# Kernel tuning notes

Hardware: AMD Instinct MI355X
Metric: run time of the kernel (lower is better)

## Reference

```python
import jax, jax.numpy as jnp
import numpy as np

LN_EPS = 1e-5


def _ssm_scan(x_ssm, A, Bm, C, reverse):
    # x_ssm: [B, L, d_inner]; A, Bm, C: [d_inner, d_state]
    Bb, L, di = x_ssm.shape
    ds = Bm.shape[1]

    def step(h, x_t):
        # h: [B, d_inner, d_state], x_t: [B, d_inner]
        h = jnp.clip(h * A[None] + x_t[:, :, None] * Bm[None], -10.0, 10.0)
        y = jnp.einsum('bid,id->bi', h, C)
        return h, y

    h0 = jnp.zeros((Bb, di, ds), x_ssm.dtype)
    _, ys = jax.lax.scan(step, h0, jnp.swapaxes(x_ssm, 0, 1), reverse=reverse)
    return jnp.swapaxes(ys, 0, 1)  # [B, L, d_inner], time-ordered


def setup_inputs() -> dict:
    key = jax.random.key(0)
    ks = jax.random.split(key, 6)
    B, L, D = 4, 2048, 1024
    d_state, expand = 16, 2
    d_inner = D * expand
    x = jax.random.normal(ks[0], (B, L, D), jnp.float32)
    # xavier-ish scaled params
    in_proj_w = jax.random.normal(ks[1], (d_inner * 2, D), jnp.float32) * np.float32(1.0 / np.sqrt(D))
    A_log = jax.random.normal(ks[2], (d_inner, d_state), jnp.float32)
    B_mat = jax.random.normal(ks[3], (d_inner, d_state), jnp.float32) * np.float32(1.0 / np.sqrt(d_state))
    C_mat = jnp.full((d_inner, d_state), 0.01, jnp.float32)
    out_proj_w = jax.random.normal(ks[4], (D, d_inner), jnp.float32) * np.float32(1.0 / np.sqrt(d_inner))
    ln_w = jnp.ones((D,), jnp.float32)
    ln_b = jnp.zeros((D,), jnp.float32)
    return {"x": x, "in_proj_w": in_proj_w, "A_log": A_log, "B_mat": B_mat,
            "C_mat": C_mat, "out_proj_w": out_proj_w, "ln_w": ln_w, "ln_b": ln_b}


def reference(x, in_proj_w, A_log, B_mat, C_mat, out_proj_w, ln_w, ln_b):
    # LayerNorm
    mu = jnp.mean(x, axis=-1, keepdims=True)
    var = jnp.mean((x - mu) ** 2, axis=-1, keepdims=True)
    xn = (x - mu) * jax.lax.rsqrt(var + LN_EPS) * ln_w + ln_b
    # in_proj (no bias), split into ssm stream and gate
    x_proj = jnp.einsum('bld,ed->ble', xn, in_proj_w)  # [B, L, 2*d_inner]
    x_ssm, gate = jnp.split(x_proj, 2, axis=-1)
    # A = -clamp(exp(A_log), -10, -0.01)  (saturates to 0.01, kept faithfully)
    A = -jnp.clip(jnp.exp(A_log), -10.0, -0.01)
    out_f = _ssm_scan(x_ssm, A, B_mat, C_mat, reverse=False)
    out_b = _ssm_scan(x_ssm, A, B_mat, C_mat, reverse=True)
    out = (out_f + out_b) * 0.5 * jax.nn.silu(gate)
    return jnp.einsum('bli,di->bld', out, out_proj_w)
```

## Files before the change

### kernel.cpp

```cpp
#include <hip/hip_runtime.h>

typedef __attribute__((ext_vector_type(8))) _Float16 f16x8;
typedef __attribute__((ext_vector_type(4))) float f32x4;

#define GLOBAL_AS __attribute__((address_space(1)))
#define LDS_AS __attribute__((address_space(3)))

static constexpr int Bb = 4, LL = 2048, DD = 1024, DI = 2048, DS = 16;
static constexpr int MROWS = Bb * LL;
static constexpr int N1 = 2 * DI;
static constexpr int K1 = DD;
static constexpr int N2 = DD;
static constexpr int K2 = DI;

__device__ __forceinline__ unsigned short f2h(float f) {
  _Float16 h = (_Float16)f;
  union { _Float16 h; unsigned short u; } c; c.h = h;
  return c.u;
}
__device__ __forceinline__ float h2f(unsigned short u) {
  union { unsigned short u; _Float16 h; } c; c.u = u;
  return (float)c.h;
}

__global__ __launch_bounds__(256) void ln_half_kernel(
    const float* __restrict__ x, const float* __restrict__ lnw,
    const float* __restrict__ lnb, unsigned short* __restrict__ A1) {
  const int r = blockIdx.x;
  const int tid = threadIdx.x;
  const float4 v = reinterpret_cast<const float4*>(x + (size_t)r * DD)[tid];
  float s = v.x + v.y + v.z + v.w;
#pragma unroll
  for (int off = 32; off >= 1; off >>= 1) s += __shfl_xor(s, off, 64);
  __shared__ float red[8];
  const int wid = tid >> 6;
  if ((tid & 63) == 0) red[wid] = s;
  __syncthreads();
  const float mu = (red[0] + red[1] + red[2] + red[3]) * (1.0f / DD);
  const float dx = v.x - mu, dy = v.y - mu, dz = v.z - mu, dw = v.w - mu;
  float ss = dx * dx + dy * dy + dz * dz + dw * dw;
#pragma unroll
  for (int off = 32; off >= 1; off >>= 1) ss += __shfl_xor(ss, off, 64);
  if ((tid & 63) == 0) red[4 + wid] = ss;
  __syncthreads();
  const float var = (red[4] + red[5] + red[6] + red[7]) * (1.0f / DD);
  const float rs = rsqrtf(var + 1e-5f);
  const float4 w4 = reinterpret_cast<const float4*>(lnw)[tid];
  const float4 b4 = reinterpret_cast<const float4*>(lnb)[tid];
  ushort4 h4;
  h4.x = f2h(dx * rs * w4.x + b4.x);
  h4.y = f2h(dy * rs * w4.y + b4.y);
  h4.z = f2h(dz * rs * w4.z + b4.z);
  h4.w = f2h(dw * rs * w4.w + b4.w);
  *reinterpret_cast<ushort4*>(&A1[(size_t)r * DD + tid * 4]) = h4;
}

__global__ __launch_bounds__(256) void f32_to_f16_kernel(
    const float* __restrict__ W, unsigned short* __restrict__ O) {
  const int gid = blockIdx.x * 256 + threadIdx.x;
  const float4 w = reinterpret_cast<const float4*>(W)[gid];
  ushort4 h4;
  h4.x = f2h(w.x); h4.y = f2h(w.y); h4.z = f2h(w.z); h4.w = f2h(w.w);
  reinterpret_cast<ushort4*>(O)[gid] = h4;
}

__global__ __launch_bounds__(512, 2) void gemm_bt_256(
    const unsigned short* __restrict__ A, const unsigned short* __restrict__ B,
    unsigned short* __restrict__ C, int M, int N, int K) {
  __shared__ unsigned short sm[2][2][256 * 64];
  const int tid = threadIdx.x;
  const int wid = tid >> 6;
  const int lane = tid & 63;
  const int wm = wid >> 2;
  const int wn = wid & 3;
  const int mt = M >> 8;
  const int cpx = gridDim.x >> 3;
  const int bid = blockIdx.x;
  const int sw = (bid & 7) * cpx + (bid >> 3);
  const int bm = sw % mt;
  const int bn = sw / mt;
  const size_t arow0 = (size_t)bm * 256;
  const size_t brow0 = (size_t)bn * 256;

  const unsigned short* gA[4];
  const unsigned short* gB[4];
#pragma unroll
  for (int j = 0; j < 4; ++j) {
    const int idx = j * 512 + tid;
    const int prow = idx >> 3;
    const int scol = ((idx & 7) ^ (prow & 7)) << 3;
    gA[j] = A + (arow0 + prow) * (size_t)K + scol;
    gB[j] = B + (brow0 + prow) * (size_t)K + scol;
  }
  auto stageA = [&](int buf) {
#pragma unroll
    for (int j = 0; j < 4; ++j) {
      __builtin_amdgcn_global_load_lds((const GLOBAL_AS void*)gA[j],
          (LDS_AS void*)&sm[buf][0][(j * 512 + (wid << 6)) * 8], 16, 0, 0);
      gA[j] += 64;
    }
  };
  auto stageB = [&](int buf) {
#pragma unroll
    for (int j = 0; j < 4; ++j) {
      __builtin_amdgcn_global_load_lds((const GLOBAL_AS void*)gB[j],
          (LDS_AS void*)&sm[buf][1][(j * 512 + (wid << 6)) * 8], 16, 0, 0);
      gB[j] += 64;
    }
  };

  const int q = lane >> 4;
  const int l7 = lane & 7;
  const int fr = lane & 15;
  int swz[2];
  swz[0] = (q << 3) ^ (l7 << 3);
  swz[1] = (32 + (q << 3)) ^ (l7 << 3);

  int arows[8], brows[4];
#pragma unroll
  for (int mf = 0; mf < 8; ++mf) arows[mf] = ((wm << 7) + mf * 16 + fr) * 64;
#pragma unroll
  for (int nf = 0; nf < 4; ++nf) brows[nf] = ((wn << 6) + nf * 16 + fr) * 64;

  f32x4 acc[8][4] = {};

  const int NTK = K >> 6;
  stageA(0);
  stageB(0);
  asm volatile("s_waitcnt vmcnt(0)" ::: "memory");
  __builtin_amdgcn_s_barrier();

  for (int t = 0; t < NTK; ++t) {
    const int cur = t & 1, nxt = cur ^ 1;
    const bool more = (t + 1 < NTK);
    f16x8 aF[4][2], bL[2][2], bH[2][2];
#pragma unroll
    for (int mf = 0; mf < 4; ++mf)
#pragma unroll
      for (int ks = 0; ks < 2; ++ks)
        aF[mf][ks] = *reinterpret_cast<const f16x8*>(&sm[cur][0][arows[mf] + swz[ks]]);
#pragma unroll
    for (int nf = 0; nf < 2; ++nf)
#pragma unroll
      for (int ks = 0; ks < 2; ++ks)
        bL[nf][ks] = *reinterpret_cast<const f16x8*>(&sm[cur][1][brows[nf] + swz[ks]]);
    if (more) stageA(nxt);
    __builtin_amdgcn_s_barrier();
    asm volatile("s_waitcnt lgkmcnt(0)" ::: "memory");
    __builtin_amdgcn_sched_barrier(0);
    __builtin_amdgcn_s_setprio(1);
#pragma unroll
    for (int mf = 0; mf < 4; ++mf)
#pragma unroll
      for (int nf = 0; nf < 2; ++nf)
#pragma unroll
        for (int ks = 0; ks < 2; ++ks)
          acc[mf][nf] = __builtin_amdgcn_mfma_f32_16x16x32_f16(
              aF[mf][ks], bL[nf][ks], acc[mf][nf], 0, 0, 0);
    __builtin_amdgcn_s_setprio(0);
    __builtin_amdgcn_s_barrier();
#pragma unroll
    for (int nf = 0; nf < 2; ++nf)
#pragma unroll
      for (int ks = 0; ks < 2; ++ks)
        bH[nf][ks] = *reinterpret_cast<const f16x8*>(&sm[cur][1][brows[2 + nf] + swz[ks]]);
    if (more) stageB(nxt);
    __builtin_amdgcn_s_barrier();
    asm volatile("s_waitcnt lgkmcnt(0)" ::: "memory");
    __builtin_amdgcn_sched_barrier(0);
    __builtin_amdgcn_s_setprio(1);
#pragma unroll
    for (int mf = 0; mf < 4; ++mf)
#pragma unroll
      for (int nf = 0; nf < 2; ++nf)
#pragma unroll
        for (int ks = 0; ks < 2; ++ks)
          acc[mf][2 + nf] = __builtin_amdgcn_mfma_f32_16x16x32_f16(
              aF[mf][ks], bH[nf][ks], acc[mf][2 + nf], 0, 0, 0);
    __builtin_amdgcn_s_setprio(0);
    __builtin_amdgcn_s_barrier();
#pragma unroll
    for (int mf = 0; mf < 4; ++mf)
#pragma unroll
      for (int ks = 0; ks < 2; ++ks)
        aF[mf][ks] = *reinterpret_cast<const f16x8*>(&sm[cur][0][arows[4 + mf] + swz[ks]]);
    __builtin_amdgcn_s_barrier();
    asm volatile("s_waitcnt lgkmcnt(0)" ::: "memory");
    __builtin_amdgcn_sched_barrier(0);
    __builtin_amdgcn_s_setprio(1);
#pragma unroll
    for (int mf = 0; mf < 4; ++mf)
#pragma unroll
      for (int nf = 0; nf < 2; ++nf)
#pragma unroll
        for (int ks = 0; ks < 2; ++ks)
          acc[4 + mf][2 + nf] = __builtin_amdgcn_mfma_f32_16x16x32_f16(
              aF[mf][ks], bH[nf][ks], acc[4 + mf][2 + nf], 0, 0, 0);
    __builtin_amdgcn_s_setprio(0);
    __builtin_amdgcn_s_barrier();
    __builtin_amdgcn_s_setprio(1);
#pragma unroll
    for (int mf = 0; mf < 4; ++mf)
#pragma unroll
      for (int nf = 0; nf < 2; ++nf)
#pragma unroll
        for (int ks = 0; ks < 2; ++ks)
          acc[4 + mf][nf] = __builtin_amdgcn_mfma_f32_16x16x32_f16(
              aF[mf][ks], bL[nf][ks], acc[4 + mf][nf], 0, 0, 0);
    __builtin_amdgcn_s_setprio(0);
    if (more) asm volatile("s_waitcnt vmcnt(0)" ::: "memory");
    __builtin_amdgcn_s_barrier();
  }

  const int fcol = lane & 15;
  const int frow4 = (lane >> 4) << 2;
#pragma unroll
  for (int mf = 0; mf < 8; ++mf)
#pragma unroll
    for (int nf = 0; nf < 4; ++nf) {
      const size_t row0 = arow0 + (wm << 7) + mf * 16 + frow4;
      const size_t col = brow0 + (wn << 6) + nf * 16 + fcol;
#pragma unroll
      for (int j = 0; j < 4; ++j)
        C[(row0 + j) * (size_t)N + col] = f2h(acc[mf][nf][j]);
    }
}

__global__ __launch_bounds__(256) void gemm_bt(
    const unsigned short* __restrict__ A, const unsigned short* __restrict__ B,
    float* __restrict__ C, int M, int N, int K) {
  __shared__ unsigned short lA[128 * 32];
  __shared__ unsigned short lB[128 * 32];
  const int tid = threadIdx.x;
  const int wid = tid >> 6;
  const int lane = tid & 63;
  const size_t arow0 = (size_t)blockIdx.x * 128;
  const size_t brow0 = (size_t)blockIdx.y * 128;
  const int wr = wid >> 1, wc = wid & 1;
  f32x4 acc[4][4] = {};

  const int idx0 = tid, idx1 = 256 + tid;
  const unsigned short* ga0 = A + (arow0 + (idx0 >> 2)) * K + (idx0 & 3) * 8;
  const unsigned short* ga1 = A + (arow0 + (idx1 >> 2)) * K + (idx1 & 3) * 8;
  const unsigned short* gb0 = B + (brow0 + (idx0 >> 2)) * K + (idx0 & 3) * 8;
  const unsigned short* gb1 = B + (brow0 + (idx1 >> 2)) * K + (idx1 & 3) * 8;
  const int lb0 = (wid * 64) * 8;
  const int lb1 = (256 + wid * 64) * 8;

  for (int k0 = 0; k0 < K; k0 += 32) {
    __builtin_amdgcn_global_load_lds((const GLOBAL_AS void*)(ga0 + k0),
                                     (LDS_AS void*)(&lA[lb0]), 16, 0, 0);
    __builtin_amdgcn_global_load_lds((const GLOBAL_AS void*)(ga1 + k0),
                                     (LDS_AS void*)(&lA[lb1]), 16, 0, 0);
    __builtin_amdgcn_global_load_lds((const GLOBAL_AS void*)(gb0 + k0),
                                     (LDS_AS void*)(&lB[lb0]), 16, 0, 0);
    __builtin_amdgcn_global_load_lds((const GLOBAL_AS void*)(gb1 + k0),
                                     (LDS_AS void*)(&lB[lb1]), 16, 0, 0);
    __syncthreads();
    const int fr = lane & 15;
    const int fo = (lane >> 4) * 8;
    f16x8 af[4], bfr[4];
#pragma unroll
    for (int m = 0; m < 4; ++m)
      af[m] = *reinterpret_cast<const f16x8*>(&lA[(wr * 64 + m * 16 + fr) * 32 + fo]);
#pragma unroll
    for (int n = 0; n < 4; ++n)
      bfr[n] = *reinterpret_cast<const f16x8*>(&lB[(wc * 64 + n * 16 + fr) * 32 + fo]);
#pragma unroll
    for (int m = 0; m < 4; ++m)
#pragma unroll
      for (int n = 0; n < 4; ++n)
        acc[m][n] = __builtin_amdgcn_mfma_f32_16x16x32_f16(af[m], bfr[n], acc[m][n], 0, 0, 0);
    __syncthreads();
  }
  const int fcol = lane & 15;
  const int frow = (lane >> 4) * 4;
#pragma unroll
  for (int m = 0; m < 4; ++m)
#pragma unroll
    for (int n = 0; n < 4; ++n)
#pragma unroll
      for (int j = 0; j < 4; ++j) {
        const size_t row = arow0 + wr * 64 + m * 16 + frow + j;
        const size_t col = brow0 + wc * 64 + n * 16 + fcol;
        C[row * (size_t)N + col] = acc[m][n][j];
      }
}

__global__ __launch_bounds__(256) void scan_kernel(
    const unsigned short* __restrict__ xp, const float* __restrict__ Bm,
    const float* __restrict__ Cm, unsigned short* __restrict__ oss) {
  constexpr int T = 32, KH = 8;
  const int blk = blockIdx.x;
  const int igrp = blk & 7;
  const int c = (blk >> 3) & 63;
  const int b = blk >> 9;
  const int tid = threadIdx.x;
  const int i = igrp * 256 + tid;
  float d = 0.f;
  {
    const float4* bp = reinterpret_cast<const float4*>(Bm + (size_t)i * DS);
    const float4* cp = reinterpret_cast<const float4*>(Cm + (size_t)i * DS);
#pragma unroll
    for (int qv = 0; qv < 4; ++qv) {
      const float4 bv = bp[qv], cv = cp[qv];
      d += bv.x * cv.x + bv.y * cv.y + bv.z * cv.z + bv.w * cv.w;
    }
  }
  const float dh = 0.5f * d;
  const int t0 = c * T;
  const size_t rowbase = (size_t)b * LL;
  float yf[T];
  float g = 0.f;
  {
    const int hstart = (t0 >= KH) ? t0 - KH : 0;
    for (int t = hstart; t < t0; ++t)
      g = fmaf(0.01f, g, h2f(xp[(rowbase + t) * (size_t)N1 + i]));
#pragma unroll
    for (int j = 0; j < T; ++j) {
      g = fmaf(0.01f, g, h2f(xp[(rowbase + t0 + j) * (size_t)N1 + i]));
      yf[j] = g;
    }
  }
  g = 0.f;
  {
    const int tend = (t0 + T - 1 + KH <= LL - 1) ? (t0 + T - 1 + KH) : (LL - 1);
    for (int t = tend; t >= t0 + T; --t)
      g = fmaf(0.01f, g, h2f(xp[(rowbase + t) * (size_t)N1 + i]));
#pragma unroll
    for (int j = T - 1; j >= 0; --j) {
      const size_t row = rowbase + t0 + j;
      g = fmaf(0.01f, g, h2f(xp[row * (size_t)N1 + i]));
      const float gt = h2f(xp[row * (size_t)N1 + DI + i]);
      const float sg = gt / (1.f + expf(-gt));
      const float o = (yf[j] + g) * dh * sg;
      oss[row * (size_t)DI + i] = f2h(o);
    }
  }
}

extern "C" void kernel_launch(void* const* d_in, const int* in_sizes, int n_in,
                              void* d_out, int out_size, void* d_ws, size_t ws_size,
                              hipStream_t stream) {
  (void)in_sizes; (void)n_in; (void)out_size; (void)ws_size;
  const float* x          = (const float*)d_in[0];
  const float* in_proj_w  = (const float*)d_in[1];
  const float* B_mat      = (const float*)d_in[3];
  const float* C_mat      = (const float*)d_in[4];
  const float* out_proj_w = (const float*)d_in[5];
  const float* ln_w       = (const float*)d_in[6];
  const float* ln_b       = (const float*)d_in[7];
  float* out = (float*)d_out;

  char* ws = (char*)d_ws;
  unsigned short* A1  = (unsigned short*)ws; ws += (size_t)MROWS * K1 * 2;
  unsigned short* B1  = (unsigned short*)ws; ws += (size_t)N1 * K1 * 2;
  unsigned short* B2  = (unsigned short*)ws; ws += (size_t)N2 * K2 * 2;
  unsigned short* OSS = (unsigned short*)ws; ws += (size_t)MROWS * DI * 2;
  unsigned short* XP  = (unsigned short*)ws; ws += (size_t)MROWS * N1 * 2;

  f32_to_f16_kernel<<<dim3((N1 * K1 / 4) / 256), dim3(256), 0, stream>>>(in_proj_w, B1);
  f32_to_f16_kernel<<<dim3((N2 * K2 / 4) / 256), dim3(256), 0, stream>>>(out_proj_w, B2);
  ln_half_kernel<<<dim3(MROWS), dim3(256), 0, stream>>>(x, ln_w, ln_b, A1);
  gemm_bt_256<<<dim3((MROWS / 256) * (N1 / 256)), dim3(512), 0, stream>>>(A1, B1, XP, MROWS, N1, K1);
  scan_kernel<<<dim3(2048), dim3(256), 0, stream>>>(XP, B_mat, C_mat, OSS);
  gemm_bt<<<dim3(MROWS / 128, N2 / 128), dim3(256), 0, stream>>>(OSS, B2, out, MROWS, N2, K2);
}
```

Baseline: 194.4 us.

## Replace out_proj GEMM with double-buffered 256x128 tile kernel with swizzled LDS

The output-projection GEMM moves from a simple 128x128 single-buffer kernel to a 512-thread 256x128 tile kernel. It double-buffers LDS, prefetching the next K=64 slice while MFMAs run on the current one. It also uses an XOR-swizzled LDS layout to avoid bank conflicts, staged barriers with setprio, and a swizzled block order for L2 locality. The aim is to hide global-load latency and raise MFMA utilisation, at the cost of more LDS per block and fewer blocks in flight.

Result: no change. 191.0 us (-1.7%).

```diff
diff --git a/kernel.cpp b/kernel.cpp
--- a/kernel.cpp
+++ b/kernel.cpp
@@ -226,65 +226,160 @@
     }
 }
 
-__global__ __launch_bounds__(256) void gemm_bt(
+__global__ __launch_bounds__(512, 2) void gemm_bt_256n128(
     const unsigned short* __restrict__ A, const unsigned short* __restrict__ B,
     float* __restrict__ C, int M, int N, int K) {
-  __shared__ unsigned short lA[128 * 32];
-  __shared__ unsigned short lB[128 * 32];
+  __shared__ unsigned short sm[2][24576];
   const int tid = threadIdx.x;
   const int wid = tid >> 6;
   const int lane = tid & 63;
-  const size_t arow0 = (size_t)blockIdx.x * 128;
-  const size_t brow0 = (size_t)blockIdx.y * 128;
-  const int wr = wid >> 1, wc = wid & 1;
-  f32x4 acc[4][4] = {};
-
-  const int idx0 = tid, idx1 = 256 + tid;
-  const unsigned short* ga0 = A + (arow0 + (idx0 >> 2)) * K + (idx0 & 3) * 8;
-  const unsigned short* ga1 = A + (arow0 + (idx1 >> 2)) * K + (idx1 & 3) * 8;
-  const unsigned short* gb0 = B + (brow0 + (idx0 >> 2)) * K + (idx0 & 3) * 8;
-  const unsigned short* gb1 = B + (brow0 + (idx1 >> 2)) * K + (idx1 & 3) * 8;
-  const int lb0 = (wid * 64) * 8;
-  const int lb1 = (256 + wid * 64) * 8;
-
-  for (int k0 = 0; k0 < K; k0 += 32) {
-    __builtin_amdgcn_global_load_lds((const GLOBAL_AS void*)(ga0 + k0),
-                                     (LDS_AS void*)(&lA[lb0]), 16, 0, 0);
-    __builtin_amdgcn_global_load_lds((const GLOBAL_AS void*)(ga1 + k0),
-                                     (LDS_AS void*)(&lA[lb1]), 16, 0, 0);
-    __builtin_amdgcn_global_load_lds((const GLOBAL_AS void*)(gb0 + k0),
-                                     (LDS_AS void*)(&lB[lb0]), 16, 0, 0);
-    __builtin_amdgcn_global_load_lds((const GLOBAL_AS void*)(gb1 + k0),
-                                     (LDS_AS void*)(&lB[lb1]), 16, 0, 0);
-    __syncthreads();
-    const int fr = lane & 15;
-    const int fo = (lane >> 4) * 8;
-    f16x8 af[4], bfr[4];
-#pragma unroll
-    for (int m = 0; m < 4; ++m)
-      af[m] = *reinterpret_cast<const f16x8*>(&lA[(wr * 64 + m * 16 + fr) * 32 + fo]);
-#pragma unroll
-    for (int n = 0; n < 4; ++n)
-      bfr[n] = *reinterpret_cast<const f16x8*>(&lB[(wc * 64 + n * 16 + fr) * 32 + fo]);
-#pragma unroll
-    for (int m = 0; m < 4; ++m)
-#pragma unroll
-      for (int n = 0; n < 4; ++n)
-        acc[m][n] = __builtin_amdgcn_mfma_f32_16x16x32_f16(af[m], bfr[n], acc[m][n], 0, 0, 0);
-    __syncthreads();
-  }
+  const int wm = wid >> 2;
+  const int wn = wid & 3;
+  const int mt = M >> 8;
+  const int cpx = gridDim.x >> 3;
+  const int bid = blockIdx.x;
+  const int sw = (bid & 7) * cpx + (bid >> 3);
+  const int bm = sw % mt;
+  const int bn = sw / mt;
+  const size_t arow0 = (size_t)bm * 256;
+  const size_t brow0 = (size_t)bn * 128;
+
+  const unsigned short* gA[4];
+  const unsigned short* gB[2];
+#pragma unroll
+  for (int j = 0; j < 4; ++j) {
+    const int idx = j * 512 + tid;
+    const int prow = idx >> 3;
+    const int scol = ((idx & 7) ^ (prow & 7)) << 3;
+    gA[j] = A + (arow0 + prow) * (size_t)K + scol;
+  }
+#pragma unroll
+  for (int j = 0; j < 2; ++j) {
+    const int idx = j * 512 + tid;
+    const int prow = idx >> 3;
+    const int scol = ((idx & 7) ^ (prow & 7)) << 3;
+    gB[j] = B + (brow0 + prow) * (size_t)K + scol;
+  }
+  auto stageA = [&](int buf) {
+#pragma unroll
+    for (int j = 0; j < 4; ++j) {
+      __builtin_amdgcn_global_load_lds((const GLOBAL_AS void*)gA[j],
+          (LDS_AS void*)&sm[buf][(j * 512 + (wid << 6)) * 8], 16, 0, 0);
+      gA[j] += 64;
+    }
+  };
+  auto stageB = [&](int buf) {
+#pragma unroll
+    for (int j = 0; j < 2; ++j) {
+      __builtin_amdgcn_global_load_lds((const GLOBAL_AS void*)gB[j],
+          (LDS_AS void*)&sm[buf][16384 + (j * 512 + (wid << 6)) * 8], 16, 0, 0);
+      gB[j] += 64;
+    }
+  };
+
+  const int q = lane >> 4;
+  const int l7 = lane & 7;
+  const int fr = lane & 15;
+  int swz[2];
+  swz[0] = (q << 3) ^ (l7 << 3);
+  swz[1] = (32 + (q << 3)) ^ (l7 << 3);
+
+  int arows[8], brows[2];
+#pragma unroll
+  for (int mf = 0; mf < 8; ++mf) arows[mf] = ((wm << 7) + mf * 16 + fr) * 64;
+#pragma unroll
+  for (int nf = 0; nf < 2; ++nf) brows[nf] = 16384 + ((wn << 5) + nf * 16 + fr) * 64;
+
+  f32x4 acc[8][2] = {};
+
+  const int NTK = K >> 6;
+  stageA(0);
+  stageB(0);
+  asm volatile("s_waitcnt vmcnt(0)" ::: "memory");
+  __builtin_amdgcn_s_barrier();
+
+  for (int t = 0; t < NTK; ++t) {
+    const int cur = t & 1, nxt = cur ^ 1;
+    const bool more = (t + 1 < NTK);
+    f16x8 aF[4][2], bL[2], bH[2];
+#pragma unroll
+    for (int mf = 0; mf < 4; ++mf)
+#pragma unroll
+      for (int ks = 0; ks < 2; ++ks)
+        aF[mf][ks] = *reinterpret_cast<const f16x8*>(&sm[cur][arows[mf] + swz[ks]]);
+#pragma unroll
+    for (int ks = 0; ks < 2; ++ks)
+      bL[ks] = *reinterpret_cast<const f16x8*>(&sm[cur][brows[0] + swz[ks]]);
+    if (more) stageA(nxt);
+    __builtin_amdgcn_s_barrier();
+    asm volatile("s_waitcnt lgkmcnt(0)" ::: "memory");
+    __builtin_amdgcn_sched_barrier(0);
+    __builtin_amdgcn_s_setprio(1);
+#pragma unroll
+    for (int mf = 0; mf < 4; ++mf)
+#pragma unroll
+      for (int ks = 0; ks < 2; ++ks)
+        acc[mf][0] = __builtin_amdgcn_mfma_f32_16x16x32_f16(
+            aF[mf][ks], bL[ks], acc[mf][0], 0, 0, 0);
+    __builtin_amdgcn_s_setprio(0);
+    __builtin_amdgcn_s_barrier();
+#pragma unroll
+    for (int ks = 0; ks < 2; ++ks)
+      bH[ks] = *reinterpret_cast<const f16x8*>(&sm[cur][brows[1] + swz[ks]]);
+    if (more) stageB(nxt);
+    __builtin_amdgcn_s_barrier();
+    asm volatile("s_waitcnt lgkmcnt(0)" ::: "memory");
+    __builtin_amdgcn_sched_barrier(0);
+    __builtin_amdgcn_s_setprio(1);
+#pragma unroll
+    for (int mf = 0; mf < 4; ++mf)
+#pragma unroll
+      for (int ks = 0; ks < 2; ++ks)
+        acc[mf][1] = __builtin_amdgcn_mfma_f32_16x16x32_f16(
+            aF[mf][ks], bH[ks], acc[mf][1], 0, 0, 0);
+    __builtin_amdgcn_s_setprio(0);
+    __builtin_amdgcn_s_barrier();
+#pragma unroll
+    for (int mf = 0; mf < 4; ++mf)
+#pragma unroll
+      for (int ks = 0; ks < 2; ++ks)
+        aF[mf][ks] = *reinterpret_cast<const f16x8*>(&sm[cur][arows[4 + mf] + swz[ks]]);
+    __builtin_amdgcn_s_barrier();
+    asm volatile("s_waitcnt lgkmcnt(0)" ::: "memory");
+    __builtin_amdgcn_sched_barrier(0);
+    __builtin_amdgcn_s_setprio(1);
+#pragma unroll
+    for (int mf = 0; mf < 4; ++mf)
+#pragma unroll
+      for (int ks = 0; ks < 2; ++ks)
+        acc[4 + mf][1] = __builtin_amdgcn_mfma_f32_16x16x32_f16(
+            aF[mf][ks], bH[ks], acc[4 + mf][1], 0, 0, 0);
+    __builtin_amdgcn_s_setprio(0);
+    __builtin_amdgcn_s_barrier();
+    __builtin_amdgcn_s_setprio(1);
+#pragma unroll
+    for (int mf = 0; mf < 4; ++mf)
+#pragma unroll
+      for (int ks = 0; ks < 2; ++ks)
+        acc[4 + mf][0] = __builtin_amdgcn_mfma_f32_16x16x32_f16(
+            aF[mf][ks], bL[ks], acc[4 + mf][0], 0, 0, 0);
+    __builtin_amdgcn_s_setprio(0);
+    if (more) asm volatile("s_waitcnt vmcnt(0)" ::: "memory");
+    __builtin_amdgcn_s_barrier();
+  }
+
   const int fcol = lane & 15;
-  const int frow = (lane >> 4) * 4;
-#pragma unroll
-  for (int m = 0; m < 4; ++m)
-#pragma unroll
-    for (int n = 0; n < 4; ++n)
-#pragma unroll
-      for (int j = 0; j < 4; ++j) {
-        const size_t row = arow0 + wr * 64 + m * 16 + frow + j;
-        const size_t col = brow0 + wc * 64 + n * 16 + fcol;
-        C[row * (size_t)N + col] = acc[m][n][j];
-      }
+  const int frow4 = (lane >> 4) << 2;
+#pragma unroll
+  for (int mf = 0; mf < 8; ++mf)
+#pragma unroll
+    for (int nf = 0; nf < 2; ++nf) {
+      const size_t row0 = arow0 + (wm << 7) + mf * 16 + frow4;
+      const size_t col = brow0 + (wn << 5) + nf * 16 + fcol;
+#pragma unroll
+      for (int j = 0; j < 4; ++j)
+        C[(row0 + j) * (size_t)N + col] = acc[mf][nf][j];
+    }
 }
 
 __global__ __launch_bounds__(256) void scan_kernel(
@@ -364,5 +459,5 @@
   ln_half_kernel<<<dim3(MROWS), dim3(256), 0, stream>>>(x, ln_w, ln_b, A1);
   gemm_bt_256<<<dim3((MROWS / 256) * (N1 / 256)), dim3(512), 0, stream>>>(A1, B1, XP, MROWS, N1, K1);
   scan_kernel<<<dim3(2048), dim3(256), 0, stream>>>(XP, B_mat, C_mat, OSS);
-  gemm_bt<<<dim3(MROWS / 128, N2 / 128), dim3(256), 0, stream>>>(OSS, B2, out, MROWS, N2, K2);
-}
+  gemm_bt_256n128<<<dim3((MROWS / 256) * (N2 / 128)), dim3(512), 0, stream>>>(OSS, B2, out, MROWS, N2, K2);
+}
```
